# Performance work log

Measured on AMD Instinct MI355X. Metric: run time of the kernel, lower is better.

The kernel has to match this reference:

```python
import jax, jax.numpy as jnp
import numpy as np

N, E, IN_DIM, HID, HEADS, OUT_DIM = 50000, 800000, 256, 32, 8, 64
NEG_SLOPE = 0.2  # PyG GATConv default


def segment_softmax(logits, seg, num_segments):
    # logits: [E, H], seg: [E] destination node ids. Self-loops guarantee no empty segment.
    m = jnp.full((num_segments, logits.shape[1]), -jnp.inf, logits.dtype).at[seg].max(logits)
    e = jnp.exp(logits - m[seg])
    s = jnp.zeros((num_segments, logits.shape[1]), logits.dtype).at[seg].add(e)
    return e / s[seg]


def gat_conv(x, src, dst, W, a_src, a_dst, b, heads, out_ch, concat):
    n = x.shape[0]
    h = (x @ W).reshape(n, heads, out_ch)                      # [N,H,C]
    alpha_src = jnp.einsum('nhc,hc->nh', h, a_src)             # [N,H]
    alpha_dst = jnp.einsum('nhc,hc->nh', h, a_dst)             # [N,H]
    logits = jax.nn.leaky_relu(alpha_src[src] + alpha_dst[dst], NEG_SLOPE)  # [E,H]
    alpha = segment_softmax(logits, dst, n)                    # [E,H]
    msg = alpha[:, :, None] * h[src]                           # [E,H,C]
    out = jnp.zeros((n, heads, out_ch), x.dtype).at[dst].add(msg)
    out = out.reshape(n, heads * out_ch) if concat else out.mean(axis=1)
    return out + b


def setup_inputs() -> dict:
    key = jax.random.key(0)
    ks = jax.random.split(key, 10)
    x = jax.random.normal(ks[0], (N, IN_DIM), dtype=jnp.float32)
    edge_index = jax.random.randint(ks[1], (2, E), 0, N, dtype=jnp.int64)
    s1 = 1.0 / np.sqrt(IN_DIM)
    s2 = 1.0 / np.sqrt(HID * HEADS)
    return {
        'x': x,
        'edge_index': edge_index,
        'W1': jax.random.normal(ks[2], (IN_DIM, HEADS * HID), dtype=jnp.float32) * s1,
        'a_src1': jax.random.normal(ks[3], (HEADS, HID), dtype=jnp.float32) * s1,
        'a_dst1': jax.random.normal(ks[4], (HEADS, HID), dtype=jnp.float32) * s1,
        'b1': jnp.zeros((HEADS * HID,), dtype=jnp.float32),
        'W2': jax.random.normal(ks[5], (HEADS * HID, OUT_DIM), dtype=jnp.float32) * s2,
        'a_src2': jax.random.normal(ks[6], (1, OUT_DIM), dtype=jnp.float32) * s2,
        'a_dst2': jax.random.normal(ks[7], (1, OUT_DIM), dtype=jnp.float32) * s2,
        'b2': jnp.zeros((OUT_DIM,), dtype=jnp.float32),
    }


def reference(x, edge_index, W1, a_src1, a_dst1, b1, W2, a_src2, a_dst2, b2):
    # add self-loops (PyG GATConv default add_self_loops=True)
    loops = jnp.arange(N, dtype=edge_index.dtype)
    src = jnp.concatenate([edge_index[0], loops])
    dst = jnp.concatenate([edge_index[1], loops])
    h = gat_conv(x, src, dst, W1, a_src1, a_dst1, b1, HEADS, HID, True)
    h = jax.nn.elu(h)  # dropout identity in eval mode
    out = gat_conv(h, src, dst, W2, a_src2, a_dst2, b2, 1, OUT_DIM, False)
    return out
```

## Files before the change

kernel.cpp:

```cpp
#include <hip/hip_runtime.h>
#include <hip/hip_bf16.h>

static constexpr int HEADS = 8;
static constexpr int D1 = 256;
static constexpr int ODIM = 64;
static constexpr float NEG = 0.2f;

typedef __attribute__((ext_vector_type(8))) short bf16x8;
typedef __attribute__((ext_vector_type(8))) unsigned short u16x8;
typedef __attribute__((ext_vector_type(4))) float f32x4;

__device__ __forceinline__ float lrelu(float x) { return fmaxf(x, NEG * x); }
__device__ __forceinline__ float elu1(float x) { return x > 0.f ? x : expm1f(x); }

__device__ __forceinline__ unsigned short f2bf(float f) {
  unsigned u = __float_as_uint(f);
  unsigned r = (u + 0x7fffu + ((u >> 16) & 1u)) >> 16;
  return (unsigned short)r;
}
__device__ __forceinline__ float bf2f(unsigned short h) {
  return __uint_as_float((unsigned)h << 16);
}

__device__ __forceinline__ void gload_lds16(const void* g, void* l) {
  __builtin_amdgcn_global_load_lds(
      (const __attribute__((address_space(1))) void*)g,
      (__attribute__((address_space(3))) void*)l, 16, 0, 0);
}

__global__ void k_hist_prep(const int* __restrict__ dst, int E, int TE,
                            int* __restrict__ deg,
                            const float* __restrict__ W1, const float* __restrict__ W2,
                            unsigned short* __restrict__ BT1, unsigned short* __restrict__ B2T,
                            int HB) {
  int b = blockIdx.x;
  if (b < HB) {
    int i = b * 256 + threadIdx.x;
    if (i < TE) {
      int d = (i < E) ? dst[i] : (i - E);
      atomicAdd(&deg[d], 1);
    }
  } else {
    int t = (b - HB) * 256 + threadIdx.x;
    if (t < 65536) {
      int k = t >> 8, nn = t & 255;
      BT1[nn * 256 + k] = f2bf(W1[t]);
    } else if (t < 65536 + 16384) {
      int t2 = t - 65536;
      int k = t2 >> 6, nn = t2 & 63;
      B2T[nn * 256 + k] = f2bf(W2[t2]);
    }
  }
}

__global__ void k_scan_lb(const int* __restrict__ deg, int n, int TE,
                          int* __restrict__ offs, int* __restrict__ cursor,
                          int* __restrict__ tstate, int* __restrict__ ticket) {
  __shared__ int sm[256];
  __shared__ int sh[2];
  if (threadIdx.x == 0) sh[0] = atomicAdd(ticket, 1);
  __syncthreads();
  const int tile = sh[0];
  int i = tile * 256 + threadIdx.x;
  int v = (i < n) ? deg[i] : 0;
  sm[threadIdx.x] = v;
  __syncthreads();
  for (int off = 1; off < 256; off <<= 1) {
    int t = (threadIdx.x >= off) ? sm[threadIdx.x - off] : 0;
    __syncthreads();
    sm[threadIdx.x] += t;
    __syncthreads();
  }
  const int total = sm[255];
  if (threadIdx.x == 0) {
    if (tile == 0) {
      __hip_atomic_store(&tstate[0], (2 << 24) | total, __ATOMIC_RELEASE,
                         __HIP_MEMORY_SCOPE_AGENT);
      sh[1] = 0;
    } else {
      __hip_atomic_store(&tstate[tile], (1 << 24) | total, __ATOMIC_RELEASE,
                         __HIP_MEMORY_SCOPE_AGENT);
    }
  }
  __syncthreads();
  if (tile != 0) {
    if (threadIdx.x < 64) {
      const int lane = threadIdx.x;
      int running = 0;
      int wstart = tile - 1;
      for (;;) {
        int idx = wstart - lane;
        int st = (idx >= 0)
                     ? __hip_atomic_load(&tstate[idx], __ATOMIC_ACQUIRE,
                                         __HIP_MEMORY_SCOPE_AGENT)
                     : (2 << 24);
        if (__ballot(st == 0)) continue;
        unsigned long long pref = __ballot((st >> 24) == 2);
        int contrib;
        if (pref) {
          int flane = (int)__ffsll(pref) - 1;
          contrib = (lane <= flane) ? (st & 0xFFFFFF) : 0;
        } else {
          contrib = st & 0xFFFFFF;
        }
#pragma unroll
        for (int off2 = 1; off2 < 64; off2 <<= 1) contrib += __shfl_xor(contrib, off2);
        running += contrib;
        if (pref) break;
        wstart -= 64;
      }
      if (lane == 0) {
        sh[1] = running;
        __hip_atomic_store(&tstate[tile], (2 << 24) | (running + total),
                           __ATOMIC_RELEASE, __HIP_MEMORY_SCOPE_AGENT);
      }
    }
    __syncthreads();
  }
  const int base = sh[1];
  if (i < n) {
    int o = base + sm[threadIdx.x] - v;
    offs[i] = o;
    cursor[i] = o;
  }
  if (i == 0) offs[n] = TE;
}

__global__ void k_scatter(const int* __restrict__ src, const int* __restrict__ dst,
                          int E, int TE, int* __restrict__ cursor, int* __restrict__ csr_src) {
  int i = blockIdx.x * blockDim.x + threadIdx.x;
  if (i >= TE) return;
  int s, d;
  if (i < E) { s = src[i]; d = dst[i]; } else { s = i - E; d = i - E; }
  int p = atomicAdd(&cursor[d], 1);
  csr_src[p] = s;
}

__global__ __launch_bounds__(512) void k_gemm1(
    const float* __restrict__ X,
    const unsigned short* __restrict__ BT,
    const float* __restrict__ a_src, const float* __restrict__ a_dst,
    unsigned short* __restrict__ h1b,
    float* __restrict__ asrc, float* __restrict__ adst,
    int M) {
  __shared__ __align__(128) char As[16384];
  __shared__ __align__(128) char Bs[32768];
  const int tid = threadIdx.x;
  const int lane = tid & 63;
  const int wid = tid >> 6;
  const int bm = blockIdx.x * 128;
  const int wm = wid >> 2, wn = wid & 3;
  f32x4 acc[4][4] = {};
  for (int kb = 0; kb < 256; kb += 64) {
#pragma unroll
    for (int q = 0; q < 2; ++q) {
      int c = q * 512 + tid;
      int r = c >> 3, kc = c & 7;
      int gr = bm + r;
      float4 v0 = make_float4(0.f, 0.f, 0.f, 0.f), v1 = v0;
      if (gr < M) {
        v0 = *(const float4*)&X[(size_t)gr * 256 + kb + kc * 8];
        v1 = *(const float4*)&X[(size_t)gr * 256 + kb + kc * 8 + 4];
      }
      float vv[8] = {v0.x, v0.y, v0.z, v0.w, v1.x, v1.y, v1.z, v1.w};
      u16x8 hv;
#pragma unroll
      for (int j = 0; j < 8; ++j) hv[j] = f2bf(vv[j]);
      *(u16x8*)(As + r * 128 + ((kc * 16) ^ ((r & 7) << 4))) = hv;
    }
#pragma unroll
    for (int q = 0; q < 4; ++q) {
      int c = q * 512 + tid;
      int col = c >> 3;
      int b = ((c & 7) * 16) ^ ((col & 7) << 4);
      gload_lds16(BT + (size_t)col * 256 + kb + (b >> 1),
                  Bs + (size_t)(q * 512 + (tid & ~63)) * 16);
    }
    __syncthreads();
#pragma unroll
    for (int ks = 0; ks < 2; ++ks) {
      bf16x8 af[4], bfr[4];
      int bb = ks * 64 + (lane >> 4) * 16;
#pragma unroll
      for (int mi = 0; mi < 4; ++mi) {
        int row = wm * 64 + mi * 16 + (lane & 15);
        af[mi] = *(const bf16x8*)(As + row * 128 + (bb ^ ((row & 7) << 4)));
      }
#pragma unroll
      for (int ni = 0; ni < 4; ++ni) {
        int col = wn * 64 + ni * 16 + (lane & 15);
        bfr[ni] = *(const bf16x8*)(Bs + col * 128 + (bb ^ ((col & 7) << 4)));
      }
#pragma unroll
      for (int mi = 0; mi < 4; ++mi)
#pragma unroll
        for (int ni = 0; ni < 4; ++ni)
          acc[mi][ni] = __builtin_amdgcn_mfma_f32_16x16x32_bf16(af[mi], bfr[ni],
                                                                acc[mi][ni], 0, 0, 0);
    }
    __syncthreads();
  }
  const int h0 = 2 * wn, h1h = 2 * wn + 1;
  const int cl = lane & 15;
  const float as0 = a_src[h0 * 32 + cl],      ad0 = a_dst[h0 * 32 + cl];
  const float as1 = a_src[h0 * 32 + 16 + cl], ad1 = a_dst[h0 * 32 + 16 + cl];
  const float as2 = a_src[h1h * 32 + cl],      ad2 = a_dst[h1h * 32 + cl];
  const float as3 = a_src[h1h * 32 + 16 + cl], ad3 = a_dst[h1h * 32 + 16 + cl];
#pragma unroll
  for (int mi = 0; mi < 4; ++mi) {
    int gr0 = bm + wm * 64 + mi * 16 + (lane >> 4) * 4;
#pragma unroll
    for (int j = 0; j < 4; ++j) {
      int gr = gr0 + j;
#pragma unroll
      for (int ni = 0; ni < 4; ++ni) {
        int gc = wn * 64 + ni * 16 + cl;
        if (gr < M) h1b[(size_t)gr * 256 + gc] = f2bf(acc[mi][ni][j]);
      }
      float ps0 = acc[mi][0][j] * as0 + acc[mi][1][j] * as1;
      float pd0 = acc[mi][0][j] * ad0 + acc[mi][1][j] * ad1;
      float ps1 = acc[mi][2][j] * as2 + acc[mi][3][j] * as3;
      float pd1 = acc[mi][2][j] * ad2 + acc[mi][3][j] * ad3;
#pragma unroll
      for (int off = 1; off < 16; off <<= 1) {
        ps0 += __shfl_xor(ps0, off);
        pd0 += __shfl_xor(pd0, off);
        ps1 += __shfl_xor(ps1, off);
        pd1 += __shfl_xor(pd1, off);
      }
      if (cl == 0 && gr < M) {
        asrc[gr * 8 + h0] = ps0;
        adst[gr * 8 + h0] = pd0;
        asrc[gr * 8 + h1h] = ps1;
        adst[gr * 8 + h1h] = pd1;
      }
    }
  }
}

__global__ __launch_bounds__(512) void k_gemm2(
    const unsigned short* __restrict__ A,
    const unsigned short* __restrict__ B2T,
    const float* __restrict__ a_src, const float* __restrict__ a_dst,
    unsigned short* __restrict__ C,
    float* __restrict__ asrc, float* __restrict__ adst,
    int M) {
  __shared__ __align__(128) char As[16384];
  __shared__ __align__(128) char Bs[8192];
  __shared__ float red[2][128][2];
  const int tid = threadIdx.x;
  const int lane = tid & 63;
  const int wid = tid >> 6;
  const int bm = blockIdx.x * 128;
  const int wm = wid >> 1, wn = wid & 1;
  f32x4 acc[2][2] = {};
  for (int kb = 0; kb < 256; kb += 64) {
#pragma unroll
    for (int q = 0; q < 2; ++q) {
      int c = q * 512 + tid;
      int r = c >> 3;
      int b = ((c & 7) * 16) ^ ((r & 7) << 4);
      gload_lds16(A + (size_t)(bm + r) * 256 + kb + (b >> 1),
                  As + (size_t)(q * 512 + (tid & ~63)) * 16);
    }
    {
      int c = tid;
      int col = c >> 3;
      int b = ((c & 7) * 16) ^ ((col & 7) << 4);
      gload_lds16(B2T + (size_t)col * 256 + kb + (b >> 1),
                  Bs + (size_t)(tid & ~63) * 16);
    }
    __syncthreads();
#pragma unroll
    for (int ks = 0; ks < 2; ++ks) {
      bf16x8 af[2], bfr[2];
      int bb = ks * 64 + (lane >> 4) * 16;
#pragma unroll
      for (int mi = 0; mi < 2; ++mi) {
        int row = wm * 32 + mi * 16 + (lane & 15);
        af[mi] = *(const bf16x8*)(As + row * 128 + (bb ^ ((row & 7) << 4)));
      }
#pragma unroll
      for (int ni = 0; ni < 2; ++ni) {
        int col = wn * 32 + ni * 16 + (lane & 15);
        bfr[ni] = *(const bf16x8*)(Bs + col * 128 + (bb ^ ((col & 7) << 4)));
      }
#pragma unroll
      for (int mi = 0; mi < 2; ++mi)
#pragma unroll
        for (int ni = 0; ni < 2; ++ni)
          acc[mi][ni] = __builtin_amdgcn_mfma_f32_16x16x32_bf16(af[mi], bfr[ni],
                                                                acc[mi][ni], 0, 0, 0);
    }
    __syncthreads();
  }
  const int cl = lane & 15;
  const float a_s0 = a_src[wn * 32 + cl],      a_d0 = a_dst[wn * 32 + cl];
  const float a_s1 = a_src[wn * 32 + 16 + cl], a_d1 = a_dst[wn * 32 + 16 + cl];
#pragma unroll
  for (int mi = 0; mi < 2; ++mi) {
    int rl0 = wm * 32 + mi * 16 + (lane >> 4) * 4;
#pragma unroll
    for (int j = 0; j < 4; ++j) {
      int rl = rl0 + j;
      int gr = bm + rl;
#pragma unroll
      for (int ni = 0; ni < 2; ++ni) {
        int gc = wn * 32 + ni * 16 + cl;
        if (gr < M) C[(size_t)gr * 64 + gc] = f2bf(acc[mi][ni][j]);
      }
      float ps = acc[mi][0][j] * a_s0 + acc[mi][1][j] * a_s1;
      float pd = acc[mi][0][j] * a_d0 + acc[mi][1][j] * a_d1;
#pragma unroll
      for (int off = 1; off < 16; off <<= 1) {
        ps += __shfl_xor(ps, off);
        pd += __shfl_xor(pd, off);
      }
      if (cl == 0) {
        red[wn][rl][0] = ps;
        red[wn][rl][1] = pd;
      }
    }
  }
  __syncthreads();
  if (tid < 128) {
    int gr = bm + tid;
    if (gr < M) {
      asrc[gr] = red[0][tid][0] + red[1][tid][0];
      adst[gr] = red[0][tid][1] + red[1][tid][1];
    }
  }
}

__global__ void k_agg1(const int* __restrict__ offs, const int* __restrict__ csr_src,
                       const unsigned short* __restrict__ h1b, const float* __restrict__ asrc,
                       const float* __restrict__ adst, const float* __restrict__ b1,
                       int n, unsigned short* __restrict__ helu) {
  int wave = (blockIdx.x * blockDim.x + threadIdx.x) >> 6;
  int lane = threadIdx.x & 63;
  if (wave >= n) return;
  int wv = __builtin_amdgcn_readfirstlane(wave);
  const int es = lane >> 5;
  const int cg = lane & 31;
  const int hh = cg >> 2;
  float ad = adst[wv * 8 + hh];
  int b = offs[wv], e2 = offs[wv + 1];
  float ssum = 0.f;
  float acc[8] = {};
  int i = b;
  for (; i + 7 < e2; i += 8) {
#pragma unroll
    for (int u = 0; u < 4; ++u) {
      int s = csr_src[i + 2 * u + es];
      u16x8 r = *(const u16x8*)&h1b[(size_t)s * D1 + cg * 8];
      float w = __expf(lrelu(asrc[s * 8 + hh] + ad));
      ssum += w;
#pragma unroll
      for (int j = 0; j < 8; ++j) acc[j] += w * bf2f(r[j]);
    }
  }
  for (; i < e2; i += 2) {
    int idx = i + es;
    bool act = idx < e2;
    int s = csr_src[act ? idx : e2 - 1];
    u16x8 r = *(const u16x8*)&h1b[(size_t)s * D1 + cg * 8];
    float w = act ? __expf(lrelu(asrc[s * 8 + hh] + ad)) : 0.f;
    ssum += w;
#pragma unroll
    for (int j = 0; j < 8; ++j) acc[j] += w * bf2f(r[j]);
  }
  ssum += __shfl_xor(ssum, 32);
#pragma unroll
  for (int j = 0; j < 8; ++j) acc[j] += __shfl_xor(acc[j], 32);
  if (lane < 32) {
    float rr = 1.f / ssum;
    float4 bb0 = *(const float4*)&b1[cg * 8];
    float4 bb1 = *(const float4*)&b1[cg * 8 + 4];
    float bbv[8] = {bb0.x, bb0.y, bb0.z, bb0.w, bb1.x, bb1.y, bb1.z, bb1.w};
    u16x8 o;
#pragma unroll
    for (int j = 0; j < 8; ++j) o[j] = f2bf(elu1(acc[j] * rr + bbv[j]));
    *(u16x8*)&helu[(size_t)wave * D1 + cg * 8] = o;
  }
}

__global__ void k_agg2(const int* __restrict__ offs, const int* __restrict__ csr_src,
                       const unsigned short* __restrict__ h2b, const float* __restrict__ asrc,
                       const float* __restrict__ adst, const float* __restrict__ b2,
                       int n, float* __restrict__ out) {
  int wave = (blockIdx.x * blockDim.x + threadIdx.x) >> 6;
  int lane = threadIdx.x & 63;
  if (wave >= n) return;
  int wv = __builtin_amdgcn_readfirstlane(wave);
  float ad = adst[wv];
  int b = offs[wv], e2 = offs[wv + 1];
  const int es = lane >> 3;
  const int cg = lane & 7;
  float ssum = 0.f;
  float acc[8] = {};
  int i = b;
  for (; i + 7 < e2; i += 8) {
    int s = csr_src[i + es];
    u16x8 r = *(const u16x8*)&h2b[(size_t)s * ODIM + cg * 8];
    float w = __expf(lrelu(asrc[s] + ad));
    ssum += w;
#pragma unroll
    for (int j = 0; j < 8; ++j) acc[j] += w * bf2f(r[j]);
  }
  if (i < e2) {
    int idx = i + es;
    bool act = idx < e2;
    int s = csr_src[act ? idx : e2 - 1];
    u16x8 r = *(const u16x8*)&h2b[(size_t)s * ODIM + cg * 8];
    float w = act ? __expf(lrelu(asrc[s] + ad)) : 0.f;
    ssum += w;
#pragma unroll
    for (int j = 0; j < 8; ++j) acc[j] += w * bf2f(r[j]);
  }
#pragma unroll
  for (int off = 8; off < 64; off <<= 1) {
    ssum += __shfl_xor(ssum, off);
#pragma unroll
    for (int j = 0; j < 8; ++j) acc[j] += __shfl_xor(acc[j], off);
  }
  if (lane < 8) {
    float r = 1.f / ssum;
    float4 bb0 = *(const float4*)&b2[cg * 8];
    float4 bb1 = *(const float4*)&b2[cg * 8 + 4];
    float4 o0, o1;
    o0.x = acc[0] * r + bb0.x; o0.y = acc[1] * r + bb0.y;
    o0.z = acc[2] * r + bb0.z; o0.w = acc[3] * r + bb0.w;
    o1.x = acc[4] * r + bb1.x; o1.y = acc[5] * r + bb1.y;
    o1.z = acc[6] * r + bb1.z; o1.w = acc[7] * r + bb1.w;
    *(float4*)&out[(size_t)wave * ODIM + cg * 8] = o0;
    *(float4*)&out[(size_t)wave * ODIM + cg * 8 + 4] = o1;
  }
}

extern "C" void kernel_launch(void* const* d_in, const int* in_sizes, int n_in,
                              void* d_out, int out_size, void* d_ws, size_t ws_size,
                              hipStream_t stream) {
  const float* x      = (const float*)d_in[0];
  const int* eidx     = (const int*)d_in[1];
  const float* W1     = (const float*)d_in[2];
  const float* asrc1w = (const float*)d_in[3];
  const float* adst1w = (const float*)d_in[4];
  const float* b1     = (const float*)d_in[5];
  const float* W2     = (const float*)d_in[6];
  const float* asrc2w = (const float*)d_in[7];
  const float* adst2w = (const float*)d_in[8];
  const float* b2     = (const float*)d_in[9];
  float* out = (float*)d_out;

  const int N = in_sizes[0] / D1;
  const int E = in_sizes[1] / 2;
  const int TE = E + N;
  const int* src = eidx;
  const int* dst = eidx + E;
  const int Mblk = (N + 127) / 128;
  const int Mpad = Mblk * 128;
  const int nb_n = (N + 255) / 256;
  const int nb_te = (TE + 255) / 256;

  char* ws = (char*)d_ws;
  size_t off = 0;
  auto carve = [&](size_t bytes) -> char* {
    char* p = ws + off;
    off = (off + bytes + 255) & ~(size_t)255;
    return p;
  };
  unsigned short* helu = (unsigned short*)carve((size_t)Mpad * D1 * 2);
  unsigned short* h1b  = (unsigned short*)carve((size_t)Mpad * D1 * 2);
  unsigned short* h2b  = (unsigned short*)carve((size_t)N * ODIM * 2);
  unsigned short* BT1  = (unsigned short*)carve((size_t)256 * 256 * 2);
  unsigned short* B2T2 = (unsigned short*)carve((size_t)64 * 256 * 2);
  float* asrc1 = (float*)carve((size_t)N * HEADS * 4);
  float* adst1 = (float*)carve((size_t)N * HEADS * 4);
  float* asrc2 = (float*)carve((size_t)N * 4);
  float* adst2 = (float*)carve((size_t)N * 4);
  int* zr      = (int*)carve((size_t)(N + nb_n + 64) * 4);
  int* deg     = zr;
  int* tstate  = zr + N;
  int* ticket  = zr + N + nb_n;
  int* offs    = (int*)carve((size_t)(N + 1) * 4);
  int* cursor  = (int*)carve((size_t)N * 4);
  int* csr_src = (int*)carve((size_t)TE * 4);

  hipMemsetAsync(zr, 0, (size_t)(N + nb_n + 1) * 4, stream);
  {
    const int HB = nb_te;
    const int PB = (65536 + 16384) / 256;
    k_hist_prep<<<HB + PB, 256, 0, stream>>>(dst, E, TE, deg, W1, W2, BT1, B2T2, HB);
  }
  k_scan_lb<<<nb_n, 256, 0, stream>>>(deg, N, TE, offs, cursor, tstate, ticket);
  k_scatter<<<nb_te, 256, 0, stream>>>(src, dst, E, TE, cursor, csr_src);

  k_gemm1<<<Mblk, 512, 0, stream>>>(x, BT1, asrc1w, adst1w, h1b, asrc1, adst1, N);
  k_agg1<<<(N + 3) / 4, 256, 0, stream>>>(offs, csr_src, h1b, asrc1, adst1, b1, N, helu);

  k_gemm2<<<Mblk, 512, 0, stream>>>(helu, B2T2, asrc2w, adst2w, h2b, asrc2, adst2, N);
  k_agg2<<<(N + 3) / 4, 256, 0, stream>>>(offs, csr_src, h2b, asrc2, adst2, b2, N, out);
}
```

Baseline: 241.8 us.

## Fuse CSR scatter into GEMM1 launch, prefetch X, batch gathers in aggregations

Merges the edge scatter kernel into the first GEMM launch as extra blocks, so the two independent jobs share one launch and can run concurrently. GEMM1 now loads the next X tile into registers while the MFMA work on the current tile proceeds, which overlaps global latency with compute at the cost of more registers. In agg1 all four gather loads are issued before any is consumed, and agg2 handles two edges per lane per iteration, both to keep more memory requests in flight. The cost is higher register pressure and possible occupancy loss in the fused GEMM blocks, whose 48 KB of static LDS is also reserved by the scatter blocks.

```diff
diff --git a/kernel.cpp b/kernel.cpp
--- a/kernel.cpp
+++ b/kernel.cpp
@@ -126,43 +126,56 @@
   if (i == 0) offs[n] = TE;
 }
 
-__global__ void k_scatter(const int* __restrict__ src, const int* __restrict__ dst,
-                          int E, int TE, int* __restrict__ cursor, int* __restrict__ csr_src) {
-  int i = blockIdx.x * blockDim.x + threadIdx.x;
-  if (i >= TE) return;
-  int s, d;
-  if (i < E) { s = src[i]; d = dst[i]; } else { s = i - E; d = i - E; }
-  int p = atomicAdd(&cursor[d], 1);
-  csr_src[p] = s;
-}
-
-__global__ __launch_bounds__(512) void k_gemm1(
+__global__ __launch_bounds__(512) void k_gemm1s(
     const float* __restrict__ X,
     const unsigned short* __restrict__ BT,
     const float* __restrict__ a_src, const float* __restrict__ a_dst,
     unsigned short* __restrict__ h1b,
     float* __restrict__ asrc, float* __restrict__ adst,
-    int M) {
+    int M, int Mblk,
+    const int* __restrict__ src, const int* __restrict__ dst, int E, int TE,
+    int* __restrict__ cursor, int* __restrict__ csr_src) {
   __shared__ __align__(128) char As[16384];
   __shared__ __align__(128) char Bs[32768];
+  if (blockIdx.x >= Mblk) {
+    int i = (blockIdx.x - Mblk) * 512 + threadIdx.x;
+    if (i < TE) {
+      int s, d;
+      if (i < E) { s = src[i]; d = dst[i]; } else { s = i - E; d = i - E; }
+      int p = atomicAdd(&cursor[d], 1);
+      csr_src[p] = s;
+    }
+    return;
+  }
   const int tid = threadIdx.x;
   const int lane = tid & 63;
   const int wid = tid >> 6;
   const int bm = blockIdx.x * 128;
   const int wm = wid >> 2, wn = wid & 3;
   f32x4 acc[4][4] = {};
-  for (int kb = 0; kb < 256; kb += 64) {
+  float4 xv[2][2];
+  auto loadX = [&](int kb) {
 #pragma unroll
     for (int q = 0; q < 2; ++q) {
       int c = q * 512 + tid;
       int r = c >> 3, kc = c & 7;
       int gr = bm + r;
-      float4 v0 = make_float4(0.f, 0.f, 0.f, 0.f), v1 = v0;
+      xv[q][0] = make_float4(0.f, 0.f, 0.f, 0.f);
+      xv[q][1] = xv[q][0];
       if (gr < M) {
-        v0 = *(const float4*)&X[(size_t)gr * 256 + kb + kc * 8];
-        v1 = *(const float4*)&X[(size_t)gr * 256 + kb + kc * 8 + 4];
-      }
-      float vv[8] = {v0.x, v0.y, v0.z, v0.w, v1.x, v1.y, v1.z, v1.w};
+        xv[q][0] = *(const float4*)&X[(size_t)gr * 256 + kb + kc * 8];
+        xv[q][1] = *(const float4*)&X[(size_t)gr * 256 + kb + kc * 8 + 4];
+      }
+    }
+  };
+  loadX(0);
+  for (int kb = 0; kb < 256; kb += 64) {
+#pragma unroll
+    for (int q = 0; q < 2; ++q) {
+      int c = q * 512 + tid;
+      int r = c >> 3, kc = c & 7;
+      float vv[8] = {xv[q][0].x, xv[q][0].y, xv[q][0].z, xv[q][0].w,
+                     xv[q][1].x, xv[q][1].y, xv[q][1].z, xv[q][1].w};
       u16x8 hv;
 #pragma unroll
       for (int j = 0; j < 8; ++j) hv[j] = f2bf(vv[j]);
@@ -177,6 +190,7 @@
                   Bs + (size_t)(q * 512 + (tid & ~63)) * 16);
     }
     __syncthreads();
+    if (kb + 64 < 256) loadX(kb + 64);
 #pragma unroll
     for (int ks = 0; ks < 2; ++ks) {
       bf16x8 af[4], bfr[4];
@@ -349,14 +363,22 @@
   float acc[8] = {};
   int i = b;
   for (; i + 7 < e2; i += 8) {
+    int s[4];
+#pragma unroll
+    for (int u = 0; u < 4; ++u) s[u] = csr_src[i + 2 * u + es];
+    u16x8 r[4];
+    float as_[4];
 #pragma unroll
     for (int u = 0; u < 4; ++u) {
-      int s = csr_src[i + 2 * u + es];
-      u16x8 r = *(const u16x8*)&h1b[(size_t)s * D1 + cg * 8];
-      float w = __expf(lrelu(asrc[s * 8 + hh] + ad));
+      r[u] = *(const u16x8*)&h1b[(size_t)s[u] * D1 + cg * 8];
+      as_[u] = asrc[s[u] * 8 + hh];
+    }
+#pragma unroll
+    for (int u = 0; u < 4; ++u) {
+      float w = __expf(lrelu(as_[u] + ad));
       ssum += w;
 #pragma unroll
-      for (int j = 0; j < 8; ++j) acc[j] += w * bf2f(r[j]);
+      for (int j = 0; j < 8; ++j) acc[j] += w * bf2f(r[u][j]);
     }
   }
   for (; i < e2; i += 2) {
@@ -399,15 +421,18 @@
   float ssum = 0.f;
   float acc[8] = {};
   int i = b;
-  for (; i + 7 < e2; i += 8) {
-    int s = csr_src[i + es];
-    u16x8 r = *(const u16x8*)&h2b[(size_t)s * ODIM + cg * 8];
-    float w = __expf(lrelu(asrc[s] + ad));
-    ssum += w;
-#pragma unroll
-    for (int j = 0; j < 8; ++j) acc[j] += w * bf2f(r[j]);
-  }
-  if (i < e2) {
+  for (; i + 15 < e2; i += 16) {
+    int s0 = csr_src[i + es], s1 = csr_src[i + 8 + es];
+    u16x8 r0 = *(const u16x8*)&h2b[(size_t)s0 * ODIM + cg * 8];
+    u16x8 r1 = *(const u16x8*)&h2b[(size_t)s1 * ODIM + cg * 8];
+    float a0 = asrc[s0], a1 = asrc[s1];
+    float w0 = __expf(lrelu(a0 + ad));
+    float w1 = __expf(lrelu(a1 + ad));
+    ssum += w0 + w1;
+#pragma unroll
+    for (int j = 0; j < 8; ++j) acc[j] += w0 * bf2f(r0[j]) + w1 * bf2f(r1[j]);
+  }
+  for (; i < e2; i += 8) {
     int idx = i + es;
     bool act = idx < e2;
     int s = csr_src[act ? idx : e2 - 1];
@@ -461,6 +486,7 @@
   const int Mpad = Mblk * 128;
   const int nb_n = (N + 255) / 256;
   const int nb_te = (TE + 255) / 256;
+  const int nb_sc = (TE + 511) / 512;
 
   char* ws = (char*)d_ws;
   size_t off = 0;
@@ -493,9 +519,9 @@
     k_hist_prep<<<HB + PB, 256, 0, stream>>>(dst, E, TE, deg, W1, W2, BT1, B2T2, HB);
   }
   k_scan_lb<<<nb_n, 256, 0, stream>>>(deg, N, TE, offs, cursor, tstate, ticket);
-  k_scatter<<<nb_te, 256, 0, stream>>>(src, dst, E, TE, cursor, csr_src);
-
-  k_gemm1<<<Mblk, 512, 0, stream>>>(x, BT1, asrc1w, adst1w, h1b, asrc1, adst1, N);
+
+  k_gemm1s<<<Mblk + nb_sc, 512, 0, stream>>>(x, BT1, asrc1w, adst1w, h1b, asrc1, adst1,
+                                             N, Mblk, src, dst, E, TE, cursor, csr_src);
   k_agg1<<<(N + 3) / 4, 256, 0, stream>>>(offs, csr_src, h1b, asrc1, adst1, b1, N, helu);
 
   k_gemm2<<<Mblk, 512, 0, stream>>>(helu, B2T2, asrc2w, adst2w, h2b, asrc2, adst2, N);
```

New measurement: 239.5 us. Within noise of the previous version (-0.9%).
